# Optimization experiments

Measured on AMD Instinct MI355X. Metric: run time of the kernel, lower is better.

The kernel has to match this reference:

```python
import jax, jax.numpy as jnp
import numpy as np

LN_EPS = 1e-5


def _forward(x, conv_w, conv_b, ln_w, ln_b, in_proj_w, in_proj_b, out_proj_w, out_proj_b):
    # x: (1, duration, dimensions)
    B, Dur, Dim = x.shape
    xt = jnp.transpose(x, (0, 2, 1))  # (1, Dim, Dur) -> Conv1d NCH layout
    branches = []
    for b in range(Dur):  # structural loop over the 32 conv branches (kernel size k=b+1)
        k = b + 1
        L = Dur - b  # output length duration - k + 1
        w = conv_w[b, :, :, :k]  # (Dim_out, Dim_in, k); padded taps beyond k unused
        y = jax.lax.conv_general_dilated(
            xt, w, window_strides=(1,), padding='VALID',
            dimension_numbers=('NCH', 'OIH', 'NCH'))  # (1, Dim, L)
        y = y + conv_b[b][None, :, None]
        y = jax.nn.gelu(y, approximate=False)  # torch nn.GELU default is exact erf form
        # LayerNorm(normalized_shape=[1, Dim, L]) with batch==1 normalizes the whole tensor
        mu = jnp.mean(y)
        var = jnp.var(y)  # biased, matching torch LayerNorm
        y = (y - mu) * jax.lax.rsqrt(var + LN_EPS)
        y = y * ln_w[b, :, :L][None] + ln_b[b, :, :L][None]
        branches.append(y)  # dropout is identity at inference (p=0.0)
    xc = jnp.concatenate(branches, axis=2)  # (1, Dim, T), T = Dur*(Dur+1)//2
    T = xc.shape[2]

    # nn.MultiheadAttention(embed_dim=T, num_heads=T), batch_first=False: input (L=1, N=Dim, E=T).
    # With seq_len==1, softmax over the single key is exactly 1, so attention output is
    # out_proj(v_proj(value)). value_i = x[:, i, :] broadcast over N, so every batch row of
    # output_i equals out_proj(v_proj(xc[0, i])). Summing over i (the feature loop):
    Wv = in_proj_w[2 * T:]          # (T, T) value slice of in_proj
    bv = in_proj_b[2 * T:]          # (T,)
    V = xc[0] @ Wv.T + bv           # (Dim, T): row i is v-proj of feature i
    S = V.sum(axis=0) @ out_proj_w.T + Dim * out_proj_b  # (T,)  sum over the Dim-term loop
    xa = jnp.broadcast_to(S[None, None, :], (1, Dim, T))  # identical rows, as in torch

    # x.unfold(2, Dur, 4*Dur).mean(-1)
    step = 4 * Dur
    n_w = (T - Dur) // step + 1
    idx = jnp.arange(n_w)[:, None] * step + jnp.arange(Dur)[None, :]  # (n_w, Dur)
    pooled = xa[:, :, idx].mean(-1)  # (1, Dim, n_w)
    return jnp.transpose(pooled, (0, 2, 1))  # (1, n_w, Dim)


def setup_inputs() -> dict:
    key = jax.random.key(0)
    ks = jax.random.split(key, 6)
    Dur, Dim = 32, 256
    T = Dur * (Dur + 1) // 2  # 528
    x = jax.random.normal(ks[0], (1, Dur, Dim), jnp.float32)
    conv_w = jax.random.normal(ks[1], (Dur, Dim, Dim, Dur), jnp.float32) * 0.02  # padded kernel bank
    conv_b = jax.random.normal(ks[2], (Dur, Dim), jnp.float32) * 0.02
    ln_w = jnp.ones((Dur, Dim, Dur), jnp.float32)   # branch b uses [:, :, :Dur-b]
    ln_b = jnp.zeros((Dur, Dim, Dur), jnp.float32)
    in_proj_w = jax.random.normal(ks[3], (3 * T, T), jnp.float32) * 0.02
    in_proj_b = jnp.zeros((3 * T,), jnp.float32)
    out_proj_w = jax.random.normal(ks[4], (T, T), jnp.float32) * 0.02
    out_proj_b = jnp.zeros((T,), jnp.float32)
    return {"x": x, "conv_w": conv_w, "conv_b": conv_b, "ln_w": ln_w, "ln_b": ln_b,
            "in_proj_w": in_proj_w, "in_proj_b": in_proj_b,
            "out_proj_w": out_proj_w, "out_proj_b": out_proj_b}


def reference(x, conv_w, conv_b, ln_w, ln_b, in_proj_w, in_proj_b, out_proj_w, out_proj_b):
    return _forward(x, conv_w, conv_b, ln_w, ln_b, in_proj_w, in_proj_b, out_proj_w, out_proj_b)
```

## Files before the change

### kernel.cpp

```cpp
#include <hip/hip_runtime.h>
#include <math.h>

#define DUR 32
#define DIM 256
#define TT  528

#define WS_BSUM 0
#define WS_BSQ  32
#define WS_CY   64
#define WS_CW   592
#define WS_CB   1120
#define WS_S    1648
#define WS_ZERO_FLOATS 592

__device__ __forceinline__ float gelu_exact(float v) {
    return 0.5f * v * (1.0f + erff(v * 0.70710678118654752f));
}

__device__ __forceinline__ float wave_reduce_down(float v) {
    v += __shfl_down(v, 32, 64);
    v += __shfl_down(v, 16, 64);
    v += __shfl_down(v, 8, 64);
    v += __shfl_down(v, 4, 64);
    v += __shfl_down(v, 2, 64);
    v += __shfl_down(v, 1, 64);
    return v;
}

__global__ __launch_bounds__(256) void prep_kernel(
    const float* __restrict__ lnw, const float* __restrict__ lnb,
    float* __restrict__ ws)
{
    const int bid = blockIdx.x;
    const int n = threadIdx.x;
    int b = 0, off = 0;
    while (bid >= off + (DUR - b)) { off += DUR - b; ++b; }
    const int t = bid - off;
    const float lw = lnw[((size_t)(b * DIM + n)) * DUR + t];
    const float lb = lnb[((size_t)(b * DIM + n)) * DUR + t];
    __shared__ float rw[4], rb[4];
    const int wave = n >> 6, lane = n & 63;
    const float a = wave_reduce_down(lw);
    const float c = wave_reduce_down(lb);
    if (lane == 0) { rw[wave] = a; rb[wave] = c; }
    __syncthreads();
    if (n == 0) {
        ws[WS_CW + bid] = rw[0] + rw[1] + rw[2] + rw[3];
        ws[WS_CB + bid] = rb[0] + rb[1] + rb[2] + rb[3];
    }
}

template<int BB>
__device__ __forceinline__ void wave_body(
    const int o, const int lane,
    const float* __restrict__ x, const float* __restrict__ W,
    const float* __restrict__ convb, const float* __restrict__ lnw,
    float* __restrict__ ws)
{
    constexpr int k  = BB + 1;
    constexpr int L  = DUR - BB;
    constexpr int K4 = (k + 3) / 4;

    const float* Wo = W + (size_t)(BB * DIM + o) * (DIM * DUR);

    float acc[L];
#pragma unroll
    for (int t = 0; t < L; ++t) acc[t] = 0.f;

#pragma unroll 1
    for (int c = 0; c < 4; ++c) {
        const int i = c * 64 + lane;
        float4 w4[K4];
        const float* Wl = Wo + i * DUR;
#pragma unroll
        for (int m = 0; m < K4; ++m) w4[m] = *(const float4*)(Wl + 4 * m);
        float xv[32];
#pragma unroll
        for (int tau = 0; tau < 32; ++tau) xv[tau] = x[tau * DIM + i];
#pragma unroll
        for (int t = 0; t < L; ++t) {
#pragma unroll
            for (int m = 0; m < K4; ++m) {
                acc[t] = fmaf(xv[t + 4*m + 0], w4[m].x, acc[t]);
                if (4*m + 1 < k) acc[t] = fmaf(xv[t + 4*m + 1], w4[m].y, acc[t]);
                if (4*m + 2 < k) acc[t] = fmaf(xv[t + 4*m + 2], w4[m].z, acc[t]);
                if (4*m + 3 < k) acc[t] = fmaf(xv[t + 4*m + 3], w4[m].w, acc[t]);
            }
        }
    }

    float mine = 0.f;
#pragma unroll
    for (int t = 0; t < L; ++t) {
        float v = acc[t];
        v += __shfl_xor(v, 1, 64);
        v += __shfl_xor(v, 2, 64);
        v += __shfl_xor(v, 4, 64);
        v += __shfl_xor(v, 8, 64);
        v += __shfl_xor(v, 16, 64);
        v += __shfl_xor(v, 32, 64);
        if (lane == t) mine = v;
    }

    constexpr int tg = BB * DUR - (BB * (BB - 1)) / 2;
    float g = 0.f;
    if (lane < L) {
        const float y = mine + convb[BB * DIM + o];
        g = gelu_exact(y);
        const float lw = lnw[((size_t)(BB * DIM + o)) * DUR + lane];
        atomicAdd(ws + WS_CY + tg + lane, g * lw);
    }
    const float s1 = wave_reduce_down(g);
    const float s2 = wave_reduce_down(g * g);
    if (lane == 0) {
        atomicAdd(ws + WS_BSUM + BB, s1);
        atomicAdd(ws + WS_BSQ  + BB, s2);
    }
}

__global__ __launch_bounds__(256, 4) void conv_kernel(
    const float* __restrict__ x, const float* __restrict__ W,
    const float* __restrict__ convb, const float* __restrict__ lnw,
    float* __restrict__ ws)
{
    const int q    = blockIdx.x * 4 + (threadIdx.x >> 6);
    const int lane = threadIdx.x & 63;
    const int bb   = 31 - (q & 31);
    const int o    = q >> 5;
    switch (bb) {
        case  0: wave_body< 0>(o, lane, x, W, convb, lnw, ws); break;
        case  1: wave_body< 1>(o, lane, x, W, convb, lnw, ws); break;
        case  2: wave_body< 2>(o, lane, x, W, convb, lnw, ws); break;
        case  3: wave_body< 3>(o, lane, x, W, convb, lnw, ws); break;
        case  4: wave_body< 4>(o, lane, x, W, convb, lnw, ws); break;
        case  5: wave_body< 5>(o, lane, x, W, convb, lnw, ws); break;
        case  6: wave_body< 6>(o, lane, x, W, convb, lnw, ws); break;
        case  7: wave_body< 7>(o, lane, x, W, convb, lnw, ws); break;
        case  8: wave_body< 8>(o, lane, x, W, convb, lnw, ws); break;
        case  9: wave_body< 9>(o, lane, x, W, convb, lnw, ws); break;
        case 10: wave_body<10>(o, lane, x, W, convb, lnw, ws); break;
        case 11: wave_body<11>(o, lane, x, W, convb, lnw, ws); break;
        case 12: wave_body<12>(o, lane, x, W, convb, lnw, ws); break;
        case 13: wave_body<13>(o, lane, x, W, convb, lnw, ws); break;
        case 14: wave_body<14>(o, lane, x, W, convb, lnw, ws); break;
        case 15: wave_body<15>(o, lane, x, W, convb, lnw, ws); break;
        case 16: wave_body<16>(o, lane, x, W, convb, lnw, ws); break;
        case 17: wave_body<17>(o, lane, x, W, convb, lnw, ws); break;
        case 18: wave_body<18>(o, lane, x, W, convb, lnw, ws); break;
        case 19: wave_body<19>(o, lane, x, W, convb, lnw, ws); break;
        case 20: wave_body<20>(o, lane, x, W, convb, lnw, ws); break;
        case 21: wave_body<21>(o, lane, x, W, convb, lnw, ws); break;
        case 22: wave_body<22>(o, lane, x, W, convb, lnw, ws); break;
        case 23: wave_body<23>(o, lane, x, W, convb, lnw, ws); break;
        case 24: wave_body<24>(o, lane, x, W, convb, lnw, ws); break;
        case 25: wave_body<25>(o, lane, x, W, convb, lnw, ws); break;
        case 26: wave_body<26>(o, lane, x, W, convb, lnw, ws); break;
        case 27: wave_body<27>(o, lane, x, W, convb, lnw, ws); break;
        case 28: wave_body<28>(o, lane, x, W, convb, lnw, ws); break;
        case 29: wave_body<29>(o, lane, x, W, convb, lnw, ws); break;
        case 30: wave_body<30>(o, lane, x, W, convb, lnw, ws); break;
        default: wave_body<31>(o, lane, x, W, convb, lnw, ws); break;
    }
}

__global__ __launch_bounds__(256) void proj1_kernel(
    float* ws, const float* __restrict__ in_proj_w,
    const float* __restrict__ in_proj_b)
{
    __shared__ float cc[TT];
    __shared__ float mu_s[32], r_s[32];
    __shared__ int map[TT];
    const int n = threadIdx.x;
    if (n < 32) {
        const int Lb = 32 - n;
        const float cnt = 256.f * (float)Lb;
        const float mu = ws[WS_BSUM + n] / cnt;
        const float var = ws[WS_BSQ + n] / cnt - mu * mu;
        mu_s[n] = mu;
        r_s[n] = rsqrtf(var + 1e-5f);
        const int off = n * 32 - (n * (n - 1)) / 2;
        for (int t = 0; t < Lb; ++t) map[off + t] = n;
    }
    __syncthreads();
    for (int t = n; t < TT; t += 256) {
        const int b = map[t];
        cc[t] = (ws[WS_CY + t] - mu_s[b] * ws[WS_CW + t]) * r_s[b] + ws[WS_CB + t];
    }
    __syncthreads();
    const int wave = n >> 6, lane = n & 63;
    const int row = blockIdx.x * 4 + wave;
    const float* Wr = in_proj_w + (size_t)(2 * TT + row) * TT;
    float a = 0.f;
    for (int t = lane; t < TT; t += 64) a = fmaf(Wr[t], cc[t], a);
    a = wave_reduce_down(a);
    if (lane == 0) ws[WS_S + row] = a + 256.f * in_proj_b[2 * TT + row];
}

__global__ __launch_bounds__(256) void proj2_kernel(
    const float* __restrict__ ws, const float* __restrict__ out_proj_w,
    const float* __restrict__ out_proj_b, float* __restrict__ out)
{
    const int w = blockIdx.x, n = threadIdx.x;
    const int wave = n >> 6, lane = n & 63;
    __shared__ float s2s[32];
    __shared__ float mv;
    for (int jj = 0; jj < 8; ++jj) {
        const int j = wave * 8 + jj;
        const int u = w * 128 + j;
        const float* Or = out_proj_w + (size_t)u * TT;
        float a = 0.f;
        for (int t = lane; t < TT; t += 64) a = fmaf(Or[t], ws[WS_S + t], a);
        a = wave_reduce_down(a);
        if (lane == 0) s2s[j] = a + 256.f * out_proj_b[u];
    }
    __syncthreads();
    if (n < 64) {
        float v = (n < 32) ? s2s[n] : 0.f;
        v += __shfl_down(v, 16, 64);
        v += __shfl_down(v, 8, 64);
        v += __shfl_down(v, 4, 64);
        v += __shfl_down(v, 2, 64);
        v += __shfl_down(v, 1, 64);
        if (n == 0) mv = v * (1.0f / 32.0f);
    }
    __syncthreads();
    out[w * 256 + n] = mv;
}

extern "C" void kernel_launch(void* const* d_in, const int* in_sizes, int n_in,
                              void* d_out, int out_size, void* d_ws, size_t ws_size,
                              hipStream_t stream)
{
    const float* x   = (const float*)d_in[0];
    const float* W   = (const float*)d_in[1];
    const float* cb  = (const float*)d_in[2];
    const float* lnw = (const float*)d_in[3];
    const float* lnb = (const float*)d_in[4];
    const float* ipw = (const float*)d_in[5];
    const float* ipb = (const float*)d_in[6];
    const float* opw = (const float*)d_in[7];
    const float* opb = (const float*)d_in[8];
    float* ws  = (float*)d_ws;
    float* out = (float*)d_out;

    hipMemsetAsync(ws, 0, WS_ZERO_FLOATS * sizeof(float), stream);
    prep_kernel<<<TT, 256, 0, stream>>>(lnw, lnb, ws);
    conv_kernel<<<2048, 256, 0, stream>>>(x, W, cb, lnw, ws);
    proj1_kernel<<<132, 256, 0, stream>>>(ws, ipw, ipb);
    proj2_kernel<<<4, 256, 0, stream>>>(ws, opw, opb, out);
}
```

Before: 476.2 us.

## Fuse prep into conv kernel, double-buffer weight loads, remap branch-to-block assignment

The LayerNorm weight/bias column-sum prep kernel is merged into the conv kernel as extra trailing blocks, which removes one launch. The conv loop over input-channel chunks is now fully unrolled, and the next chunk's weights are prefetched into a second register buffer so global loads overlap the FMAs. Empty asm barriers pin the loaded values. Each block now runs a single branch size across 4 output channels, chosen with a scrambled mapping, where before every wave in a block had a different branch; this balances load across CUs. The double buffer and full unroll raise register pressure under the 4-blocks-per-SM launch bound.

```diff
diff --git a/kernel.cpp b/kernel.cpp
--- a/kernel.cpp
+++ b/kernel.cpp
@@ -27,29 +27,6 @@
     return v;
 }
 
-__global__ __launch_bounds__(256) void prep_kernel(
-    const float* __restrict__ lnw, const float* __restrict__ lnb,
-    float* __restrict__ ws)
-{
-    const int bid = blockIdx.x;
-    const int n = threadIdx.x;
-    int b = 0, off = 0;
-    while (bid >= off + (DUR - b)) { off += DUR - b; ++b; }
-    const int t = bid - off;
-    const float lw = lnw[((size_t)(b * DIM + n)) * DUR + t];
-    const float lb = lnb[((size_t)(b * DIM + n)) * DUR + t];
-    __shared__ float rw[4], rb[4];
-    const int wave = n >> 6, lane = n & 63;
-    const float a = wave_reduce_down(lw);
-    const float c = wave_reduce_down(lb);
-    if (lane == 0) { rw[wave] = a; rb[wave] = c; }
-    __syncthreads();
-    if (n == 0) {
-        ws[WS_CW + bid] = rw[0] + rw[1] + rw[2] + rw[3];
-        ws[WS_CB + bid] = rb[0] + rb[1] + rb[2] + rb[3];
-    }
-}
-
 template<int BB>
 __device__ __forceinline__ void wave_body(
     const int o, const int lane,
@@ -63,28 +40,44 @@
 
     const float* Wo = W + (size_t)(BB * DIM + o) * (DIM * DUR);
 
+    float4 wbuf[2][K4];
+    {
+        const float* Wl = Wo + (size_t)lane * DUR;
+#pragma unroll
+        for (int m = 0; m < K4; ++m) wbuf[0][m] = *(const float4*)(Wl + 4 * m);
+    }
+
     float acc[L];
 #pragma unroll
     for (int t = 0; t < L; ++t) acc[t] = 0.f;
 
-#pragma unroll 1
+#pragma unroll
     for (int c = 0; c < 4; ++c) {
+        const int cur = c & 1, nxt = cur ^ 1;
+        if (c < 3) {
+            const float* Wl = Wo + (size_t)((c + 1) * 64 + lane) * DUR;
+#pragma unroll
+            for (int m = 0; m < K4; ++m) wbuf[nxt][m] = *(const float4*)(Wl + 4 * m);
+        }
         const int i = c * 64 + lane;
-        float4 w4[K4];
-        const float* Wl = Wo + i * DUR;
-#pragma unroll
-        for (int m = 0; m < K4; ++m) w4[m] = *(const float4*)(Wl + 4 * m);
         float xv[32];
 #pragma unroll
         for (int tau = 0; tau < 32; ++tau) xv[tau] = x[tau * DIM + i];
 #pragma unroll
+        for (int tau = 0; tau < 32; ++tau) asm volatile("" : "+v"(xv[tau]));
+#pragma unroll
+        for (int m = 0; m < K4; ++m) {
+            asm volatile("" : "+v"(wbuf[cur][m].x), "+v"(wbuf[cur][m].y),
+                              "+v"(wbuf[cur][m].z), "+v"(wbuf[cur][m].w));
+        }
+#pragma unroll
         for (int t = 0; t < L; ++t) {
 #pragma unroll
             for (int m = 0; m < K4; ++m) {
-                acc[t] = fmaf(xv[t + 4*m + 0], w4[m].x, acc[t]);
-                if (4*m + 1 < k) acc[t] = fmaf(xv[t + 4*m + 1], w4[m].y, acc[t]);
-                if (4*m + 2 < k) acc[t] = fmaf(xv[t + 4*m + 2], w4[m].z, acc[t]);
-                if (4*m + 3 < k) acc[t] = fmaf(xv[t + 4*m + 3], w4[m].w, acc[t]);
+                acc[t] = fmaf(xv[t + 4*m + 0], wbuf[cur][m].x, acc[t]);
+                if (4*m + 1 < k) acc[t] = fmaf(xv[t + 4*m + 1], wbuf[cur][m].y, acc[t]);
+                if (4*m + 2 < k) acc[t] = fmaf(xv[t + 4*m + 2], wbuf[cur][m].z, acc[t]);
+                if (4*m + 3 < k) acc[t] = fmaf(xv[t + 4*m + 3], wbuf[cur][m].w, acc[t]);
             }
         }
     }
@@ -121,12 +114,33 @@
 __global__ __launch_bounds__(256, 4) void conv_kernel(
     const float* __restrict__ x, const float* __restrict__ W,
     const float* __restrict__ convb, const float* __restrict__ lnw,
-    float* __restrict__ ws)
-{
-    const int q    = blockIdx.x * 4 + (threadIdx.x >> 6);
-    const int lane = threadIdx.x & 63;
-    const int bb   = 31 - (q & 31);
-    const int o    = q >> 5;
+    const float* __restrict__ lnb, float* __restrict__ ws)
+{
+    const int bid = blockIdx.x;
+    const int n = threadIdx.x;
+    if (bid >= 2048) {
+        const int pb = bid - 2048;
+        int b = 0, off = 0;
+        while (pb >= off + (DUR - b)) { off += DUR - b; ++b; }
+        const int t = pb - off;
+        const float lw = lnw[((size_t)(b * DIM + n)) * DUR + t];
+        const float lb = lnb[((size_t)(b * DIM + n)) * DUR + t];
+        __shared__ float rw[4], rb[4];
+        const int wave = n >> 6, lane = n & 63;
+        const float a = wave_reduce_down(lw);
+        const float c = wave_reduce_down(lb);
+        if (lane == 0) { rw[wave] = a; rb[wave] = c; }
+        __syncthreads();
+        if (n == 0) {
+            ws[WS_CW + pb] = rw[0] + rw[1] + rw[2] + rw[3];
+            ws[WS_CB + pb] = rb[0] + rb[1] + rb[2] + rb[3];
+        }
+        return;
+    }
+
+    const int bb   = (13 * ((bid & 31) + (bid >> 8))) & 31;
+    const int o    = (bid >> 5) * 4 + (n >> 6);
+    const int lane = n & 63;
     switch (bb) {
         case  0: wave_body< 0>(o, lane, x, W, convb, lnw, ws); break;
         case  1: wave_body< 1>(o, lane, x, W, convb, lnw, ws); break;
@@ -244,8 +258,7 @@
     float* out = (float*)d_out;
 
     hipMemsetAsync(ws, 0, WS_ZERO_FLOATS * sizeof(float), stream);
-    prep_kernel<<<TT, 256, 0, stream>>>(lnw, lnb, ws);
-    conv_kernel<<<2048, 256, 0, stream>>>(x, W, cb, lnw, ws);
+    conv_kernel<<<2048 + TT, 256, 0, stream>>>(x, W, cb, lnw, lnb, ws);
     proj1_kernel<<<132, 256, 0, stream>>>(ws, ipw, ipb);
     proj2_kernel<<<4, 256, 0, stream>>>(ws, opw, opb, out);
 }
```

Result: faster. 451.8 us (-5.1%).

## Tile conv outputs by 8, drop atomics, fold LN stats into proj1

Applied to the files above, without the earlier changes.

The conv kernel now processes outputs in chunks of 8 timesteps, with templates keyed on K4 buckets instead of one per branch. This cuts register pressure and the number of code variants. Each block now holds one branch and a contiguous group of four output channels, interleaved across branches. Gelu outputs are written to a full 256x528 buffer instead of atomically accumulating LayerNorm statistics. The prep kernel and memset are removed, and the column reductions (sum, sum of squares, ln-weighted sums) move into every proj1 block, which rereads the 540KB buffer plus ln weights 132 times redundantly. Chunking also recomputes zero-padded taps and reloads the weights per chunk.

```diff
diff --git a/kernel.cpp b/kernel.cpp
--- a/kernel.cpp
+++ b/kernel.cpp
@@ -5,13 +5,8 @@
 #define DIM 256
 #define TT  528
 
-#define WS_BSUM 0
-#define WS_BSQ  32
-#define WS_CY   64
-#define WS_CW   592
-#define WS_CB   1120
-#define WS_S    1648
-#define WS_ZERO_FLOATS 592
+#define WS_G    0
+#define WS_S    (256*TT)
 
 __device__ __forceinline__ float gelu_exact(float v) {
     return 0.5f * v * (1.0f + erff(v * 0.70710678118654752f));
@@ -27,177 +22,156 @@
     return v;
 }
 
-__global__ __launch_bounds__(256) void prep_kernel(
-    const float* __restrict__ lnw, const float* __restrict__ lnb,
-    float* __restrict__ ws)
-{
-    const int bid = blockIdx.x;
-    const int n = threadIdx.x;
-    int b = 0, off = 0;
-    while (bid >= off + (DUR - b)) { off += DUR - b; ++b; }
-    const int t = bid - off;
-    const float lw = lnw[((size_t)(b * DIM + n)) * DUR + t];
-    const float lb = lnb[((size_t)(b * DIM + n)) * DUR + t];
-    __shared__ float rw[4], rb[4];
-    const int wave = n >> 6, lane = n & 63;
-    const float a = wave_reduce_down(lw);
-    const float c = wave_reduce_down(lb);
-    if (lane == 0) { rw[wave] = a; rb[wave] = c; }
-    __syncthreads();
-    if (n == 0) {
-        ws[WS_CW + bid] = rw[0] + rw[1] + rw[2] + rw[3];
-        ws[WS_CB + bid] = rb[0] + rb[1] + rb[2] + rb[3];
-    }
-}
-
-template<int BB>
+template<int K4>
 __device__ __forceinline__ void wave_body(
-    const int o, const int lane,
+    const int bb, const int o, const int lane,
     const float* __restrict__ x, const float* __restrict__ W,
-    const float* __restrict__ convb, const float* __restrict__ lnw,
-    float* __restrict__ ws)
-{
-    constexpr int k  = BB + 1;
-    constexpr int L  = DUR - BB;
-    constexpr int K4 = (k + 3) / 4;
-
-    const float* Wo = W + (size_t)(BB * DIM + o) * (DIM * DUR);
-
-    float acc[L];
-#pragma unroll
-    for (int t = 0; t < L; ++t) acc[t] = 0.f;
-
+    const float* __restrict__ convb, float* __restrict__ gbuf)
+{
+    const int k = bb + 1;
+    const int L = DUR - bb;
+    constexpr int XN = 4 * K4 + 7;
+
+    const float* Wo = W + (size_t)(bb * DIM + o) * (DIM * DUR);
+
+    float mine = 0.f;
+    const int nT8 = (L + 7) >> 3;
 #pragma unroll 1
-    for (int c = 0; c < 4; ++c) {
-        const int i = c * 64 + lane;
-        float4 w4[K4];
-        const float* Wl = Wo + i * DUR;
-#pragma unroll
-        for (int m = 0; m < K4; ++m) w4[m] = *(const float4*)(Wl + 4 * m);
-        float xv[32];
-#pragma unroll
-        for (int tau = 0; tau < 32; ++tau) xv[tau] = x[tau * DIM + i];
-#pragma unroll
-        for (int t = 0; t < L; ++t) {
+    for (int t8 = 0; t8 < nT8; ++t8) {
+        const int t0 = t8 * 8;
+        float acc[8];
+#pragma unroll
+        for (int j = 0; j < 8; ++j) acc[j] = 0.f;
+
+#pragma unroll 1
+        for (int c = 0; c < 4; ++c) {
+            const int i = c * 64 + lane;
+            const float* Wl = Wo + (size_t)i * DUR;
+            float4 w4[K4];
+#pragma unroll
+            for (int m = 0; m < K4; ++m) w4[m] = *(const float4*)(Wl + 4 * m);
 #pragma unroll
             for (int m = 0; m < K4; ++m) {
-                acc[t] = fmaf(xv[t + 4*m + 0], w4[m].x, acc[t]);
-                if (4*m + 1 < k) acc[t] = fmaf(xv[t + 4*m + 1], w4[m].y, acc[t]);
-                if (4*m + 2 < k) acc[t] = fmaf(xv[t + 4*m + 2], w4[m].z, acc[t]);
-                if (4*m + 3 < k) acc[t] = fmaf(xv[t + 4*m + 3], w4[m].w, acc[t]);
+                if (4 * m + 1 >= k) w4[m].y = 0.f;
+                if (4 * m + 2 >= k) w4[m].z = 0.f;
+                if (4 * m + 3 >= k) w4[m].w = 0.f;
+            }
+            float xv[XN];
+#pragma unroll
+            for (int j = 0; j < XN; ++j) {
+                int tau = t0 + j; tau = (tau < 31) ? tau : 31;
+                xv[j] = x[tau * DIM + i];
+            }
+#pragma unroll
+            for (int j = 0; j < 8; ++j) {
+#pragma unroll
+                for (int m = 0; m < K4; ++m) {
+                    acc[j] = fmaf(xv[j + 4*m + 0], w4[m].x, acc[j]);
+                    acc[j] = fmaf(xv[j + 4*m + 1], w4[m].y, acc[j]);
+                    acc[j] = fmaf(xv[j + 4*m + 2], w4[m].z, acc[j]);
+                    acc[j] = fmaf(xv[j + 4*m + 3], w4[m].w, acc[j]);
+                }
             }
         }
-    }
-
-    float mine = 0.f;
-#pragma unroll
-    for (int t = 0; t < L; ++t) {
-        float v = acc[t];
-        v += __shfl_xor(v, 1, 64);
-        v += __shfl_xor(v, 2, 64);
-        v += __shfl_xor(v, 4, 64);
-        v += __shfl_xor(v, 8, 64);
-        v += __shfl_xor(v, 16, 64);
-        v += __shfl_xor(v, 32, 64);
-        if (lane == t) mine = v;
-    }
-
-    constexpr int tg = BB * DUR - (BB * (BB - 1)) / 2;
-    float g = 0.f;
+#pragma unroll
+        for (int j = 0; j < 8; ++j) {
+            float v = acc[j];
+            v += __shfl_xor(v, 1, 64);
+            v += __shfl_xor(v, 2, 64);
+            v += __shfl_xor(v, 4, 64);
+            v += __shfl_xor(v, 8, 64);
+            v += __shfl_xor(v, 16, 64);
+            v += __shfl_xor(v, 32, 64);
+            if (lane == t0 + j) mine = v;
+        }
+    }
+
+    const int tg = bb * DUR - (bb * (bb - 1)) / 2;
     if (lane < L) {
-        const float y = mine + convb[BB * DIM + o];
-        g = gelu_exact(y);
-        const float lw = lnw[((size_t)(BB * DIM + o)) * DUR + lane];
-        atomicAdd(ws + WS_CY + tg + lane, g * lw);
-    }
-    const float s1 = wave_reduce_down(g);
-    const float s2 = wave_reduce_down(g * g);
-    if (lane == 0) {
-        atomicAdd(ws + WS_BSUM + BB, s1);
-        atomicAdd(ws + WS_BSQ  + BB, s2);
+        const float g = gelu_exact(mine + convb[bb * DIM + o]);
+        gbuf[(size_t)o * TT + tg + lane] = g;
     }
 }
 
 __global__ __launch_bounds__(256, 4) void conv_kernel(
     const float* __restrict__ x, const float* __restrict__ W,
-    const float* __restrict__ convb, const float* __restrict__ lnw,
-    float* __restrict__ ws)
-{
-    const int q    = blockIdx.x * 4 + (threadIdx.x >> 6);
+    const float* __restrict__ convb, float* __restrict__ ws)
+{
+    const int bid = blockIdx.x;
+    const int bb   = (13 * ((bid & 31) + (bid >> 8))) & 31;
+    const int o    = (bid >> 5) * 4 + (threadIdx.x >> 6);
     const int lane = threadIdx.x & 63;
-    const int bb   = 31 - (q & 31);
-    const int o    = q >> 5;
-    switch (bb) {
-        case  0: wave_body< 0>(o, lane, x, W, convb, lnw, ws); break;
-        case  1: wave_body< 1>(o, lane, x, W, convb, lnw, ws); break;
-        case  2: wave_body< 2>(o, lane, x, W, convb, lnw, ws); break;
-        case  3: wave_body< 3>(o, lane, x, W, convb, lnw, ws); break;
-        case  4: wave_body< 4>(o, lane, x, W, convb, lnw, ws); break;
-        case  5: wave_body< 5>(o, lane, x, W, convb, lnw, ws); break;
-        case  6: wave_body< 6>(o, lane, x, W, convb, lnw, ws); break;
-        case  7: wave_body< 7>(o, lane, x, W, convb, lnw, ws); break;
-        case  8: wave_body< 8>(o, lane, x, W, convb, lnw, ws); break;
-        case  9: wave_body< 9>(o, lane, x, W, convb, lnw, ws); break;
-        case 10: wave_body<10>(o, lane, x, W, convb, lnw, ws); break;
-        case 11: wave_body<11>(o, lane, x, W, convb, lnw, ws); break;
-        case 12: wave_body<12>(o, lane, x, W, convb, lnw, ws); break;
-        case 13: wave_body<13>(o, lane, x, W, convb, lnw, ws); break;
-        case 14: wave_body<14>(o, lane, x, W, convb, lnw, ws); break;
-        case 15: wave_body<15>(o, lane, x, W, convb, lnw, ws); break;
-        case 16: wave_body<16>(o, lane, x, W, convb, lnw, ws); break;
-        case 17: wave_body<17>(o, lane, x, W, convb, lnw, ws); break;
-        case 18: wave_body<18>(o, lane, x, W, convb, lnw, ws); break;
-        case 19: wave_body<19>(o, lane, x, W, convb, lnw, ws); break;
-        case 20: wave_body<20>(o, lane, x, W, convb, lnw, ws); break;
-        case 21: wave_body<21>(o, lane, x, W, convb, lnw, ws); break;
-        case 22: wave_body<22>(o, lane, x, W, convb, lnw, ws); break;
-        case 23: wave_body<23>(o, lane, x, W, convb, lnw, ws); break;
-        case 24: wave_body<24>(o, lane, x, W, convb, lnw, ws); break;
-        case 25: wave_body<25>(o, lane, x, W, convb, lnw, ws); break;
-        case 26: wave_body<26>(o, lane, x, W, convb, lnw, ws); break;
-        case 27: wave_body<27>(o, lane, x, W, convb, lnw, ws); break;
-        case 28: wave_body<28>(o, lane, x, W, convb, lnw, ws); break;
-        case 29: wave_body<29>(o, lane, x, W, convb, lnw, ws); break;
-        case 30: wave_body<30>(o, lane, x, W, convb, lnw, ws); break;
-        default: wave_body<31>(o, lane, x, W, convb, lnw, ws); break;
+    float* gbuf = ws + WS_G;
+    switch (bb >> 2) {
+        case 0:  wave_body<1>(bb, o, lane, x, W, convb, gbuf); break;
+        case 1:  wave_body<2>(bb, o, lane, x, W, convb, gbuf); break;
+        case 2:  wave_body<3>(bb, o, lane, x, W, convb, gbuf); break;
+        case 3:  wave_body<4>(bb, o, lane, x, W, convb, gbuf); break;
+        case 4:  wave_body<5>(bb, o, lane, x, W, convb, gbuf); break;
+        case 5:  wave_body<6>(bb, o, lane, x, W, convb, gbuf); break;
+        case 6:  wave_body<7>(bb, o, lane, x, W, convb, gbuf); break;
+        default: wave_body<8>(bb, o, lane, x, W, convb, gbuf); break;
     }
 }
 
 __global__ __launch_bounds__(256) void proj1_kernel(
-    float* ws, const float* __restrict__ in_proj_w,
-    const float* __restrict__ in_proj_b)
-{
-    __shared__ float cc[TT];
+    const float* __restrict__ ws_g, float* __restrict__ ws_s,
+    const float* __restrict__ lnw, const float* __restrict__ lnb,
+    const float* __restrict__ in_proj_w, const float* __restrict__ in_proj_b)
+{
+    __shared__ float cyr[TT], cwv[TT], cbv[TT], gs1[TT], gs2[TT];
     __shared__ float mu_s[32], r_s[32];
-    __shared__ int map[TT];
     const int n = threadIdx.x;
+
+    for (int t = n; t < TT; t += 256) {
+        int b = 0, off = 0;
+        while (t >= off + (DUR - b)) { off += DUR - b; ++b; }
+        const int tt = t - off;
+        const float* lw = lnw + (size_t)b * DIM * DUR + tt;
+        const float* lb = lnb + (size_t)b * DIM * DUR + tt;
+        const float* gp = ws_g + t;
+        float a_cy = 0.f, a_cw = 0.f, a_cb = 0.f, a_s1 = 0.f, a_s2 = 0.f;
+#pragma unroll 4
+        for (int o = 0; o < 256; ++o) {
+            const float g = gp[(size_t)o * TT];
+            const float w = lw[(size_t)o * DUR];
+            a_cy = fmaf(g, w, a_cy);
+            a_cw += w;
+            a_cb += lb[(size_t)o * DUR];
+            a_s1 += g;
+            a_s2 = fmaf(g, g, a_s2);
+        }
+        cyr[t] = a_cy; cwv[t] = a_cw; cbv[t] = a_cb; gs1[t] = a_s1; gs2[t] = a_s2;
+    }
+    __syncthreads();
     if (n < 32) {
-        const int Lb = 32 - n;
+        const int b = n, Lb = DUR - b;
+        const int off = b * DUR - (b * (b - 1)) / 2;
+        float s1 = 0.f, s2 = 0.f;
+        for (int t = 0; t < Lb; ++t) { s1 += gs1[off + t]; s2 += gs2[off + t]; }
         const float cnt = 256.f * (float)Lb;
-        const float mu = ws[WS_BSUM + n] / cnt;
-        const float var = ws[WS_BSQ + n] / cnt - mu * mu;
+        const float mu = s1 / cnt;
         mu_s[n] = mu;
-        r_s[n] = rsqrtf(var + 1e-5f);
-        const int off = n * 32 - (n * (n - 1)) / 2;
-        for (int t = 0; t < Lb; ++t) map[off + t] = n;
+        r_s[n] = rsqrtf(s2 / cnt - mu * mu + 1e-5f);
     }
     __syncthreads();
     for (int t = n; t < TT; t += 256) {
-        const int b = map[t];
-        cc[t] = (ws[WS_CY + t] - mu_s[b] * ws[WS_CW + t]) * r_s[b] + ws[WS_CB + t];
+        int b = 0, off = 0;
+        while (t >= off + (DUR - b)) { off += DUR - b; ++b; }
+        cyr[t] = (cyr[t] - mu_s[b] * cwv[t]) * r_s[b] + cbv[t];
     }
     __syncthreads();
     const int wave = n >> 6, lane = n & 63;
     const int row = blockIdx.x * 4 + wave;
     const float* Wr = in_proj_w + (size_t)(2 * TT + row) * TT;
     float a = 0.f;
-    for (int t = lane; t < TT; t += 64) a = fmaf(Wr[t], cc[t], a);
+    for (int t = lane; t < TT; t += 64) a = fmaf(Wr[t], cyr[t], a);
     a = wave_reduce_down(a);
-    if (lane == 0) ws[WS_S + row] = a + 256.f * in_proj_b[2 * TT + row];
+    if (lane == 0) ws_s[row] = a + 256.f * in_proj_b[2 * TT + row];
 }
 
 __global__ __launch_bounds__(256) void proj2_kernel(
-    const float* __restrict__ ws, const float* __restrict__ out_proj_w,
+    const float* __restrict__ ws_s, const float* __restrict__ out_proj_w,
     const float* __restrict__ out_proj_b, float* __restrict__ out)
 {
     const int w = blockIdx.x, n = threadIdx.x;
@@ -209,7 +183,7 @@
         const int u = w * 128 + j;
         const float* Or = out_proj_w + (size_t)u * TT;
         float a = 0.f;
-        for (int t = lane; t < TT; t += 64) a = fmaf(Or[t], ws[WS_S + t], a);
+        for (int t = lane; t < TT; t += 64) a = fmaf(Or[t], ws_s[t], a);
         a = wave_reduce_down(a);
         if (lane == 0) s2s[j] = a + 256.f * out_proj_b[u];
     }
@@ -243,9 +217,7 @@
     float* ws  = (float*)d_ws;
     float* out = (float*)d_out;
 
-    hipMemsetAsync(ws, 0, WS_ZERO_FLOATS * sizeof(float), stream);
-    prep_kernel<<<TT, 256, 0, stream>>>(lnw, lnb, ws);
-    conv_kernel<<<2048, 256, 0, stream>>>(x, W, cb, lnw, ws);
-    proj1_kernel<<<132, 256, 0, stream>>>(ws, ipw, ipb);
-    proj2_kernel<<<4, 256, 0, stream>>>(ws, opw, opb, out);
-}
+    conv_kernel<<<2048, 256, 0, stream>>>(x, W, cb, ws);
+    proj1_kernel<<<132, 256, 0, stream>>>(ws + WS_G, ws + WS_S, lnw, lnb, ipw, ipb);
+    proj2_kernel<<<4, 256, 0, stream>>>(ws + WS_S, opw, opb, out);
+}
```

Result: slower. 559.6 us (+17.5%).
